# Kernel tuning notes

Measured on AMD Instinct MI355X. Metric: run time of the kernel, lower is better.

Reference implementation:

```python
import jax, jax.numpy as jnp
import numpy as np

EMBED_DIM = 1024
NUM_HEADS = 16
HEAD_DIM = EMBED_DIM // NUM_HEADS
SCALE = HEAD_DIM ** -0.5


def setup_inputs() -> dict:
    key = jax.random.key(0)
    ks = jax.random.split(key, 9)
    B, N, C = 4, 2048, EMBED_DIM
    w_std = C ** -0.5
    return {
        "x": jax.random.normal(ks[0], (B, N, C), dtype=jnp.float32),
        "w_q": jax.random.normal(ks[1], (C, C), dtype=jnp.float32) * w_std,
        "b_q": jax.random.normal(ks[2], (C,), dtype=jnp.float32) * 0.02,
        "w_k": jax.random.normal(ks[3], (C, C), dtype=jnp.float32) * w_std,
        "b_k": jax.random.normal(ks[4], (C,), dtype=jnp.float32) * 0.02,
        "w_v": jax.random.normal(ks[5], (C, C), dtype=jnp.float32) * w_std,
        "b_v": jax.random.normal(ks[6], (C,), dtype=jnp.float32) * 0.02,
        "w_o": jax.random.normal(ks[7], (C, C), dtype=jnp.float32) * w_std,
        "b_o": jax.random.normal(ks[8], (C,), dtype=jnp.float32) * 0.02,
    }


def reference(x, w_q, b_q, w_k, b_k, w_v, b_v, w_o, b_o):
    B, N, C = x.shape
    H, D = NUM_HEADS, HEAD_DIM
    # qkv projections (nn.Linear: x @ W^T + b); weights stored as (out, in) -> use W directly as (in,out) by generating square random; math identical
    q = (x @ w_q + b_q).reshape(B, N, H, D).transpose(0, 2, 1, 3)  # bhnd
    k = (x @ w_k + b_k).reshape(B, N, H, D).transpose(0, 2, 1, 3)
    v = (x @ w_v + b_v).reshape(B, N, H, D).transpose(0, 2, 1, 3)
    attn = jnp.einsum("bhnd,bhmd->bhnm", q, k) * SCALE
    attn = jax.nn.softmax(attn, axis=-1)  # dropout p=0.0 -> identity
    out = jnp.einsum("bhnm,bhmd->bhnd", attn, v)
    out = out.transpose(0, 2, 1, 3).reshape(B, N, C)
    return out @ w_o + b_o
```

## Files before the change

kernel.cpp:

```cpp
#include <hip/hip_runtime.h>
#include <math.h>

constexpr float SOFTMAX_OFF = 6.0f;
constexpr float LOG2E = 1.44269504088896f;

using half2v = __attribute__((ext_vector_type(2))) _Float16;
using half4  = __attribute__((ext_vector_type(4))) _Float16;
using half8  = __attribute__((ext_vector_type(8))) _Float16;
using floatx4 = __attribute__((ext_vector_type(4))) float;

__device__ __forceinline__ void gll16(const _Float16* src, _Float16* dst) {
  __builtin_amdgcn_global_load_lds((const __attribute__((address_space(1))) void*)src,
                                   (__attribute__((address_space(3))) void*)dst, 16, 0, 0);
}
__device__ __forceinline__ float exp2_fast(float x) {
#if __has_builtin(__builtin_amdgcn_exp2f)
  return __builtin_amdgcn_exp2f(x);
#else
  float r; asm("v_exp_f32 %0, %1" : "=v"(r) : "v"(x)); return r;
#endif
}

__device__ __forceinline__ int gsw(int row) { return ((row >> 3) ^ row) & 7; }
__device__ __forceinline__ int gsw8(int row, int chunk) {
  return row * 64 + ((chunk ^ gsw(row)) << 3);
}

__device__ __forceinline__ void stage_tile(const _Float16* __restrict__ src,
                                           _Float16* lds, int tid) {
  const int w = tid >> 6, l = tid & 63;
#pragma unroll
  for (int i = 0; i < 4; i++) {
    const int rbase = w * 8 + i * 32;
    const int row = rbase + (l >> 3);
    const int chunk = (l & 7) ^ gsw(row);
    gll16(src + (size_t)row * 1024 + chunk * 8, lds + rbase * 64);
  }
}

__device__ __forceinline__ void mfma_core16(const _Float16* __restrict__ A,
                                            const _Float16* __restrict__ B,
                                            _Float16* As, _Float16* Bs,
                                            floatx4 (&acc)[4][4]) {
  const int tid = threadIdx.x;
  const int lane = tid & 63;
  const int w = tid >> 6;
  const int wrow = w >> 1, wcol = w & 1;
  const int quad = lane >> 4, lm = lane & 15;

  for (int k0 = 0; k0 < 1024; k0 += 64) {
    stage_tile(A + k0, As, tid);
    stage_tile(B + k0, Bs, tid);
    __syncthreads();

    half8 af[4][2], bf[4][2];
#pragma unroll
    for (int mi = 0; mi < 4; mi++) {
      int row = wrow * 64 + mi * 16 + lm;
      af[mi][0] = *(const half8*)&As[gsw8(row, quad)];
      af[mi][1] = *(const half8*)&As[gsw8(row, 4 + quad)];
    }
#pragma unroll
    for (int nj = 0; nj < 4; nj++) {
      int row = wcol * 64 + nj * 16 + lm;
      bf[nj][0] = *(const half8*)&Bs[gsw8(row, quad)];
      bf[nj][1] = *(const half8*)&Bs[gsw8(row, 4 + quad)];
    }
    __builtin_amdgcn_s_setprio(1);
#pragma unroll
    for (int mi = 0; mi < 4; mi++)
#pragma unroll
      for (int nj = 0; nj < 4; nj++) {
        acc[mi][nj] = __builtin_amdgcn_mfma_f32_16x16x32_f16(af[mi][0], bf[nj][0], acc[mi][nj], 0, 0, 0);
        acc[mi][nj] = __builtin_amdgcn_mfma_f32_16x16x32_f16(af[mi][1], bf[nj][1], acc[mi][nj], 0, 0, 0);
      }
    __builtin_amdgcn_s_setprio(0);
    __syncthreads();
  }
}

__global__ __launch_bounds__(256) void gemm_qkv_mfma(
    const _Float16* __restrict__ xh, const _Float16* __restrict__ WT,
    const float* __restrict__ bq, const float* __restrict__ bk, const float* __restrict__ bv,
    _Float16* __restrict__ Oq, _Float16* __restrict__ Ok, _Float16* __restrict__ Ov) {
  __shared__ __align__(16) _Float16 SM[128 * 128];
  _Float16* As = SM;
  _Float16* Bs = SM + 128 * 64;

  const int sel = blockIdx.x >> 3;
  const int colBase = (blockIdx.x & 7) * 128;
  const int rowBase = blockIdx.y * 128;
  const float* bias = (sel == 0) ? bq : (sel == 1) ? bk : bv;
  const _Float16* Bp = WT + (size_t)sel * 1048576 + (size_t)colBase * 1024;

  floatx4 acc[4][4];
#pragma unroll
  for (int mi = 0; mi < 4; mi++)
#pragma unroll
    for (int nj = 0; nj < 4; nj++) acc[mi][nj] = (floatx4){0.f, 0.f, 0.f, 0.f};

  mfma_core16(xh + (size_t)rowBase * 1024, Bp, As, Bs, acc);

  const int tid = threadIdx.x;
  const int lane = tid & 63;
  const int w = tid >> 6;
  const int wrow = w >> 1, wcol = w & 1;
  const int quad = lane >> 4, lm = lane & 15;

  if (sel < 2) {
    _Float16* out = (sel == 0) ? Oq : Ok;
#pragma unroll
    for (int nj = 0; nj < 4; nj++) {
      int col = colBase + wcol * 64 + nj * 16 + lm;
      float bv_ = bias[col];
      int h = col >> 6, d = col & 63;
#pragma unroll
      for (int mi = 0; mi < 4; mi++) {
        int row0 = rowBase + wrow * 64 + mi * 16 + quad * 4;
#pragma unroll
        for (int r = 0; r < 4; r++) {
          int row = row0 + r;
          int bb = row >> 11, n = row & 2047;
          out[((size_t)((bb * 16 + h) * 2048 + n)) * 64 + d] = (_Float16)(acc[mi][nj][r] + bv_);
        }
      }
    }
  } else {
#pragma unroll
    for (int nj = 0; nj < 4; nj++) {
      int colp = wcol * 64 + nj * 16 + lm;
      float bv_ = bias[colBase + colp];
#pragma unroll
      for (int mi = 0; mi < 4; mi++) {
        int row0 = wrow * 64 + mi * 16 + quad * 4;
#pragma unroll
        for (int r = 0; r < 4; r++) {
          int rowp = row0 + r;
          SM[colp * 128 + ((((rowp >> 3) ^ (colp & 15))) << 3) + (rowp & 7)] =
              (_Float16)(acc[mi][nj][r] + bv_);
        }
      }
    }
    __syncthreads();
    const int b = rowBase >> 11, n0 = rowBase & 2047;
    const int ci = tid & 15;
#pragma unroll
    for (int i = 0; i < 8; i++) {
      int c = (tid >> 4) * 8 + i;
      half8 hv = *(const half8*)&SM[c * 128 + ((ci ^ (c & 15)) << 3)];
      int col = colBase + c;
      int hh = col >> 6, d = col & 63;
      *(half8*)&Ov[((size_t)(b * 16 + hh) * 64 + d) * 2048 + n0 + ci * 8] = hv;
    }
  }
}

__global__ __launch_bounds__(256) void gemm_out_mfma(const _Float16* __restrict__ A,
                                                     const _Float16* __restrict__ WT,
                                                     const float* __restrict__ bias,
                                                     float* __restrict__ out) {
  __shared__ __align__(16) _Float16 SM[128 * 128];
  _Float16* As = SM;
  _Float16* Bs = SM + 128 * 64;

  const int colBase = blockIdx.x * 128;
  const int rowBase = blockIdx.y * 128;

  floatx4 acc[4][4];
#pragma unroll
  for (int mi = 0; mi < 4; mi++)
#pragma unroll
    for (int nj = 0; nj < 4; nj++) acc[mi][nj] = (floatx4){0.f, 0.f, 0.f, 0.f};

  mfma_core16(A + (size_t)rowBase * 1024, WT + (size_t)colBase * 1024, As, Bs, acc);

  const int tid = threadIdx.x;
  const int lane = tid & 63;
  const int w = tid >> 6;
  const int wrow = w >> 1, wcol = w & 1;
  const int quad = lane >> 4, lm = lane & 15;

#pragma unroll
  for (int nj = 0; nj < 4; nj++) {
    int col = colBase + wcol * 64 + nj * 16 + lm;
    float bv_ = bias[col];
#pragma unroll
    for (int mi = 0; mi < 4; mi++) {
      int row0 = rowBase + wrow * 64 + mi * 16 + quad * 4;
#pragma unroll
      for (int r = 0; r < 4; r++)
        out[(size_t)(row0 + r) * 1024 + col] = acc[mi][nj][r] + bv_;
    }
  }
}

__global__ __launch_bounds__(256) void prepass(const float* __restrict__ x,
                                               const float* __restrict__ w_q,
                                               const float* __restrict__ w_k,
                                               const float* __restrict__ w_v,
                                               _Float16* __restrict__ xh,
                                               _Float16* __restrict__ WTqkv) {
  const int bx = blockIdx.x;
  const int tid = threadIdx.x;
  if (bx < 768) {
    __shared__ float tile[64][65];
    const int wsel = bx >> 8, t = bx & 255;
    const float* W = (wsel == 0) ? w_q : (wsel == 1) ? w_k : w_v;
    _Float16* out = WTqkv + (size_t)wsel * 1048576;
    const int n0 = (t & 15) * 64, k0 = (t >> 4) * 64;
#pragma unroll
    for (int i = 0; i < 16; i++) {
      int idx = tid + i * 256;
      int r = idx >> 6, c = idx & 63;
      tile[r][c] = W[(size_t)(k0 + r) * 1024 + n0 + c];
    }
    __syncthreads();
#pragma unroll
    for (int i = 0; i < 4; i++) {
      int r = (tid >> 4) + i * 16;
      int c0 = (tid & 15) * 4;
      half4 h = {(_Float16)tile[c0][r], (_Float16)tile[c0 + 1][r],
                 (_Float16)tile[c0 + 2][r], (_Float16)tile[c0 + 3][r]};
      *(half4*)&out[(size_t)(n0 + r) * 1024 + k0 + c0] = h;
    }
  } else {
    int idx = ((bx - 768) * 256 + tid) * 8;
    float4 a = *(const float4*)(x + idx);
    float4 b = *(const float4*)(x + idx + 4);
    half8 h = {(_Float16)a.x, (_Float16)a.y, (_Float16)a.z, (_Float16)a.w,
               (_Float16)b.x, (_Float16)b.y, (_Float16)b.z, (_Float16)b.w};
    *(half8*)(xh + idx) = h;
  }
}

__global__ __launch_bounds__(256) void transpose_wo(const float* __restrict__ W,
                                                    _Float16* __restrict__ out) {
  __shared__ float tile[64][65];
  const int n0 = blockIdx.x * 64, k0 = blockIdx.y * 64;
  const int tid = threadIdx.x;
#pragma unroll
  for (int i = 0; i < 16; i++) {
    int idx = tid + i * 256;
    int r = idx >> 6, c = idx & 63;
    tile[r][c] = W[(size_t)(k0 + r) * 1024 + n0 + c];
  }
  __syncthreads();
#pragma unroll
  for (int i = 0; i < 4; i++) {
    int r = (tid >> 4) + i * 16;
    int c0 = (tid & 15) * 4;
    half4 h = {(_Float16)tile[c0][r], (_Float16)tile[c0 + 1][r],
               (_Float16)tile[c0 + 2][r], (_Float16)tile[c0 + 3][r]};
    *(half4*)&out[(size_t)(n0 + r) * 1024 + k0 + c0] = h;
  }
}

__device__ __forceinline__ int sw8(int row, int chunk) {
  return row * 64 + ((chunk ^ (row & 7)) << 3);
}

__global__ __launch_bounds__(256, 3) void flash_attn_mfma(const _Float16* __restrict__ Q,
                                                          const _Float16* __restrict__ K,
                                                          const _Float16* __restrict__ VT,
                                                          _Float16* __restrict__ out) {
  __shared__ __align__(16) _Float16 QPs[128 * 64];
  __shared__ __align__(16) _Float16 Ks[2 * 64 * 64];
  __shared__ __align__(16) _Float16 Vs[2 * 64 * 64];

  const int tid = threadIdx.x;
  const int lane = tid & 63;
  const int w = tid >> 6;
  const int quad = lane >> 4, lm = lane & 15;
  const int bh = blockIdx.y;
  const int qbase = blockIdx.x * 128;
  const int b = bh >> 4, h = bh & 15;

  const _Float16* Qp = Q + ((size_t)bh * 2048 + qbase) * 64;
  const _Float16* Kp = K + (size_t)bh * 2048 * 64;
  const _Float16* VTp = VT + (size_t)bh * 2048 * 64;

  const int soff = ((lane & 7) ^ (lane >> 3)) * 8;
  const int srow = w * 8 + (lane >> 3);

#pragma unroll
  for (int i = 0; i < 4; i++)
    gll16(Qp + (size_t)(srow + 32 * i) * 64 + soff, QPs + (w * 8 + 32 * i) * 64);
  const _Float16* kptr = Kp + srow * 64 + soff;
  const _Float16* vptr = VTp + srow * 2048 + soff;
  gll16(kptr, Ks + (w * 8) * 64);
  gll16(kptr + 32 * 64, Ks + (w * 8 + 32) * 64);
  gll16(vptr, Vs + (w * 8) * 64);
  gll16(vptr + 32 * 2048, Vs + (w * 8 + 32) * 64);
  kptr += 64 * 64;
  vptr += 64;
  __syncthreads();

  half8 aq[2][2];
#pragma unroll
  for (int s = 0; s < 2; s++) {
    aq[s][0] = *(const half8*)&QPs[sw8(32 * w + 16 * s + lm, quad)];
    aq[s][1] = *(const half8*)&QPs[sw8(32 * w + 16 * s + lm, 4 + quad)];
  }

  floatx4 o_acc[2][4];
  floatx4 l_acc[2];
#pragma unroll
  for (int s = 0; s < 2; s++) {
    l_acc[s] = (floatx4){0.f, 0.f, 0.f, 0.f};
#pragma unroll
    for (int dt = 0; dt < 4; dt++) o_acc[s][dt] = (floatx4){0.f, 0.f, 0.f, 0.f};
  }
  const half4 vone = {(_Float16)1.f, (_Float16)1.f, (_Float16)1.f, (_Float16)1.f};

  constexpr float SCL = 0.125f * LOG2E;
  constexpr float OFFC = -SOFTMAX_OFF * LOG2E;

  int voff[4][4];
#pragma unroll
  for (int dt = 0; dt < 4; dt++)
#pragma unroll
    for (int t = 0; t < 4; t++) {
      int row = 16 * dt + lm;
      voff[dt][t] = row * 64 + (((2 * t + (quad >> 1)) ^ (row & 7)) << 3) + (quad & 1) * 4;
    }

  int cur = 0;
  for (int kt = 0; kt < 32; kt++) {
    if (kt + 1 < 32) {
      _Float16* kd = Ks + (cur ^ 1) * 4096;
      _Float16* vd = Vs + (cur ^ 1) * 4096;
      gll16(kptr, kd + (w * 8) * 64);
      gll16(kptr + 32 * 64, kd + (w * 8 + 32) * 64);
      gll16(vptr, vd + (w * 8) * 64);
      gll16(vptr + 32 * 2048, vd + (w * 8 + 32) * 64);
      kptr += 64 * 64;
      vptr += 64;
    }
    const _Float16* ksC = Ks + cur * 4096;
    const _Float16* vsC = Vs + cur * 4096;

    floatx4 st[2][4];
    __builtin_amdgcn_s_setprio(1);
#pragma unroll
    for (int t = 0; t < 4; t++) {
      half8 bk0 = *(const half8*)&ksC[sw8(16 * t + lm, quad)];
      half8 bk1 = *(const half8*)&ksC[sw8(16 * t + lm, 4 + quad)];
#pragma unroll
      for (int s = 0; s < 2; s++) {
        floatx4 acc = (floatx4){0.f, 0.f, 0.f, 0.f};
        acc = __builtin_amdgcn_mfma_f32_16x16x32_f16(bk0, aq[s][0], acc, 0, 0, 0);
        acc = __builtin_amdgcn_mfma_f32_16x16x32_f16(bk1, aq[s][1], acc, 0, 0, 0);
        st[s][t] = acc;
      }
    }
    __builtin_amdgcn_s_setprio(0);

    half4 pf[2][4];
#pragma unroll
    for (int s = 0; s < 2; s++)
#pragma unroll
      for (int t = 0; t < 4; t++) {
        float p0 = exp2_fast(fmaf(st[s][t][0], SCL, OFFC));
        float p1 = exp2_fast(fmaf(st[s][t][1], SCL, OFFC));
        float p2 = exp2_fast(fmaf(st[s][t][2], SCL, OFFC));
        float p3 = exp2_fast(fmaf(st[s][t][3], SCL, OFFC));
        half2v lo = __builtin_bit_cast(half2v, __builtin_amdgcn_cvt_pkrtz(p0, p1));
        half2v hi = __builtin_bit_cast(half2v, __builtin_amdgcn_cvt_pkrtz(p2, p3));
        pf[s][t] = (half4){lo[0], lo[1], hi[0], hi[1]};
      }

    __builtin_amdgcn_s_setprio(1);
#pragma unroll
    for (int dt = 0; dt < 4; dt++) {
      half4 vf[4];
#pragma unroll
      for (int t = 0; t < 4; t++) vf[t] = *(const half4*)&vsC[voff[dt][t]];
#pragma unroll
      for (int t = 0; t < 4; t++)
#pragma unroll
        for (int s = 0; s < 2; s++)
          o_acc[s][dt] = __builtin_amdgcn_mfma_f32_16x16x16f16(vf[t], pf[s][t], o_acc[s][dt], 0, 0, 0);
    }
#pragma unroll
    for (int s = 0; s < 2; s++)
#pragma unroll
      for (int t = 0; t < 4; t++)
        l_acc[s] = __builtin_amdgcn_mfma_f32_16x16x16f16(vone, pf[s][t], l_acc[s], 0, 0, 0);
    __builtin_amdgcn_s_setprio(0);

    cur ^= 1;
    __syncthreads();
  }

#pragma unroll
  for (int s = 0; s < 2; s++) {
    float inv = 1.f / l_acc[s][0];
    int n = qbase + 32 * w + 16 * s + lm;
    _Float16* op = out + ((size_t)(b * 2048 + n)) * 1024 + h * 64 + quad * 4;
#pragma unroll
    for (int dt = 0; dt < 4; dt++) {
      half4 hv = {(_Float16)(o_acc[s][dt][0] * inv), (_Float16)(o_acc[s][dt][1] * inv),
                  (_Float16)(o_acc[s][dt][2] * inv), (_Float16)(o_acc[s][dt][3] * inv)};
      *(half4*)&op[16 * dt] = hv;
    }
  }
}

extern "C" void kernel_launch(void* const* d_in, const int* in_sizes, int n_in,
                              void* d_out, int out_size, void* d_ws, size_t ws_size,
                              hipStream_t stream) {
  const float* x   = (const float*)d_in[0];
  const float* w_q = (const float*)d_in[1];
  const float* b_q = (const float*)d_in[2];
  const float* w_k = (const float*)d_in[3];
  const float* b_k = (const float*)d_in[4];
  const float* w_v = (const float*)d_in[5];
  const float* b_v = (const float*)d_in[6];
  const float* w_o = (const float*)d_in[7];
  const float* b_o = (const float*)d_in[8];
  float* out = (float*)d_out;

  _Float16* wsh = (_Float16*)d_ws;
  _Float16* Ab = wsh;
  _Float16* Qb = wsh + 8388608;
  _Float16* Kb = wsh + 2 * 8388608;
  _Float16* Vb = wsh + 3 * 8388608;
  _Float16* xh = Ab;
  _Float16* WTqkv = (_Float16*)d_out;
  _Float16* WoT = Qb;

  dim3 blk(256);
  prepass<<<dim3(4864), blk, 0, stream>>>(x, w_q, w_k, w_v, xh, WTqkv);
  gemm_qkv_mfma<<<dim3(24, 64), blk, 0, stream>>>(xh, WTqkv, b_q, b_k, b_v, Qb, Kb, Vb);
  flash_attn_mfma<<<dim3(16, 64), blk, 0, stream>>>(Qb, Kb, Vb, Ab);
  transpose_wo<<<dim3(16, 16), blk, 0, stream>>>(w_o, WoT);
  gemm_out_mfma<<<dim3(8, 64), blk, 0, stream>>>(Ab, WoT, b_o, out);
}
```

Measured before the change: 298.8 us.

## Triple-buffer K/V tiles with partial vmcnt waits in flash attention

Switches the K/V shared-memory staging from double to triple buffering. Each iteration prefetches two tiles ahead, and a partial s_waitcnt vmcnt lets the tile one ahead stay in flight across the barrier instead of draining every global load. Launch bounds drop from 3 to 2 blocks per CU to fit the extra LDS. The intent is to hide more global-load latency, at the cost of occupancy.

```diff
diff --git a/kernel.cpp b/kernel.cpp
--- a/kernel.cpp
+++ b/kernel.cpp
@@ -259,13 +259,13 @@
   return row * 64 + ((chunk ^ (row & 7)) << 3);
 }
 
-__global__ __launch_bounds__(256, 3) void flash_attn_mfma(const _Float16* __restrict__ Q,
+__global__ __launch_bounds__(256, 2) void flash_attn_mfma(const _Float16* __restrict__ Q,
                                                           const _Float16* __restrict__ K,
                                                           const _Float16* __restrict__ VT,
                                                           _Float16* __restrict__ out) {
   __shared__ __align__(16) _Float16 QPs[128 * 64];
-  __shared__ __align__(16) _Float16 Ks[2 * 64 * 64];
-  __shared__ __align__(16) _Float16 Vs[2 * 64 * 64];
+  __shared__ __align__(16) _Float16 Ks[3 * 64 * 64];
+  __shared__ __align__(16) _Float16 Vs[3 * 64 * 64];
 
   const int tid = threadIdx.x;
   const int lane = tid & 63;
@@ -281,19 +281,29 @@
 
   const int soff = ((lane & 7) ^ (lane >> 3)) * 8;
   const int srow = w * 8 + (lane >> 3);
+  const int wb8 = w * 8;
 
 #pragma unroll
   for (int i = 0; i < 4; i++)
-    gll16(Qp + (size_t)(srow + 32 * i) * 64 + soff, QPs + (w * 8 + 32 * i) * 64);
+    gll16(Qp + (size_t)(srow + 32 * i) * 64 + soff, QPs + (wb8 + 32 * i) * 64);
   const _Float16* kptr = Kp + srow * 64 + soff;
   const _Float16* vptr = VTp + srow * 2048 + soff;
-  gll16(kptr, Ks + (w * 8) * 64);
-  gll16(kptr + 32 * 64, Ks + (w * 8 + 32) * 64);
-  gll16(vptr, Vs + (w * 8) * 64);
-  gll16(vptr + 32 * 2048, Vs + (w * 8 + 32) * 64);
+  gll16(kptr, Ks + wb8 * 64);
+  gll16(kptr + 32 * 64, Ks + (wb8 + 32) * 64);
+  gll16(vptr, Vs + wb8 * 64);
+  gll16(vptr + 32 * 2048, Vs + (wb8 + 32) * 64);
   kptr += 64 * 64;
   vptr += 64;
-  __syncthreads();
+  gll16(kptr, Ks + 4096 + wb8 * 64);
+  gll16(kptr + 32 * 64, Ks + 4096 + (wb8 + 32) * 64);
+  gll16(vptr, Vs + 4096 + wb8 * 64);
+  gll16(vptr + 32 * 2048, Vs + 4096 + (wb8 + 32) * 64);
+  kptr += 64 * 64;
+  vptr += 64;
+  asm volatile("s_waitcnt vmcnt(4)" ::: "memory");
+  __builtin_amdgcn_sched_barrier(0);
+  __builtin_amdgcn_s_barrier();
+  __builtin_amdgcn_sched_barrier(0);
 
   half8 aq[2][2];
 #pragma unroll
@@ -324,27 +334,25 @@
       voff[dt][t] = row * 64 + (((2 * t + (quad >> 1)) ^ (row & 7)) << 3) + (quad & 1) * 4;
     }
 
-  int cur = 0;
+  _Float16 *k0 = Ks, *k1 = Ks + 4096, *k2 = Ks + 8192;
+  _Float16 *v0 = Vs, *v1 = Vs + 4096, *v2 = Vs + 8192;
+
   for (int kt = 0; kt < 32; kt++) {
-    if (kt + 1 < 32) {
-      _Float16* kd = Ks + (cur ^ 1) * 4096;
-      _Float16* vd = Vs + (cur ^ 1) * 4096;
-      gll16(kptr, kd + (w * 8) * 64);
-      gll16(kptr + 32 * 64, kd + (w * 8 + 32) * 64);
-      gll16(vptr, vd + (w * 8) * 64);
-      gll16(vptr + 32 * 2048, vd + (w * 8 + 32) * 64);
+    if (kt + 2 < 32) {
+      gll16(kptr, k2 + wb8 * 64);
+      gll16(kptr + 32 * 64, k2 + (wb8 + 32) * 64);
+      gll16(vptr, v2 + wb8 * 64);
+      gll16(vptr + 32 * 2048, v2 + (wb8 + 32) * 64);
       kptr += 64 * 64;
       vptr += 64;
     }
-    const _Float16* ksC = Ks + cur * 4096;
-    const _Float16* vsC = Vs + cur * 4096;
 
     floatx4 st[2][4];
     __builtin_amdgcn_s_setprio(1);
 #pragma unroll
     for (int t = 0; t < 4; t++) {
-      half8 bk0 = *(const half8*)&ksC[sw8(16 * t + lm, quad)];
-      half8 bk1 = *(const half8*)&ksC[sw8(16 * t + lm, 4 + quad)];
+      half8 bk0 = *(const half8*)&k0[sw8(16 * t + lm, quad)];
+      half8 bk1 = *(const half8*)&k0[sw8(16 * t + lm, 4 + quad)];
 #pragma unroll
       for (int s = 0; s < 2; s++) {
         floatx4 acc = (floatx4){0.f, 0.f, 0.f, 0.f};
@@ -374,7 +382,7 @@
     for (int dt = 0; dt < 4; dt++) {
       half4 vf[4];
 #pragma unroll
-      for (int t = 0; t < 4; t++) vf[t] = *(const half4*)&vsC[voff[dt][t]];
+      for (int t = 0; t < 4; t++) vf[t] = *(const half4*)&v0[voff[dt][t]];
 #pragma unroll
       for (int t = 0; t < 4; t++)
 #pragma unroll
@@ -388,8 +396,17 @@
         l_acc[s] = __builtin_amdgcn_mfma_f32_16x16x16f16(vone, pf[s][t], l_acc[s], 0, 0, 0);
     __builtin_amdgcn_s_setprio(0);
 
-    cur ^= 1;
-    __syncthreads();
+    if (kt < 30) {
+      asm volatile("s_waitcnt vmcnt(4)" ::: "memory");
+    } else {
+      asm volatile("s_waitcnt vmcnt(0)" ::: "memory");
+    }
+    __builtin_amdgcn_sched_barrier(0);
+    __builtin_amdgcn_s_barrier();
+    __builtin_amdgcn_sched_barrier(0);
+
+    _Float16* tk = k0; k0 = k1; k1 = k2; k2 = tk;
+    _Float16* tv = v0; v0 = v1; v1 = v2; v2 = tv;
   }
 
 #pragma unroll
```

Result: no change. 294.2 us (-1.6%).
